# Kernel optimization log

Hardware: AMD Instinct MI355X
Metric: run time of the kernel (lower is better)

The kernel has to match this reference:

```python
import jax, jax.numpy as jnp
import numpy as np

B, T, I, H = 256, 512, 64, 256


def _lstm_layer(x, Wih, Whh, bih, bhh):
    # x: [B, T, in], Wih: [4H, in], Whh: [4H, H], biases: [4H]
    # PyTorch gate order: i, f, g, o.  c' = f*c + i*g ; h = o*tanh(c')
    Hd = Whh.shape[1]
    xp = jnp.einsum('bti,gi->btg', x, Wih) + bih + bhh  # [B, T, 4H]
    h0 = jnp.zeros((x.shape[0], Hd), x.dtype)
    c0 = jnp.zeros((x.shape[0], Hd), x.dtype)

    def step(carry, xt):
        h, c = carry
        g = xt + h @ Whh.T
        i, f, gg, o = jnp.split(g, 4, axis=-1)
        i = jax.nn.sigmoid(i)
        f = jax.nn.sigmoid(f)
        gg = jnp.tanh(gg)
        o = jax.nn.sigmoid(o)
        c = f * c + i * gg
        h = o * jnp.tanh(c)
        return (h, c), h

    _, hs = jax.lax.scan(step, (h0, c0), jnp.swapaxes(xp, 0, 1))  # [T, B, H]
    return jnp.swapaxes(hs, 0, 1)


def setup_inputs() -> dict:
    key = jax.random.key(0)
    ks = jax.random.split(key, 20)
    s_in = 1.0 / np.sqrt(I)
    s_h = 1.0 / np.sqrt(H)
    d = {
        'x': jax.random.normal(ks[0], (B, T, I), jnp.float32),
        # encoder layer 0: input I -> H
        'enc_Wih0': jax.random.normal(ks[1], (4 * H, I), jnp.float32) * s_in,
        'enc_Whh0': jax.random.normal(ks[2], (4 * H, H), jnp.float32) * s_h,
        'enc_bih0': jnp.zeros((4 * H,), jnp.float32),
        'enc_bhh0': jnp.zeros((4 * H,), jnp.float32),
        # encoder layer 1: H -> H
        'enc_Wih1': jax.random.normal(ks[3], (4 * H, H), jnp.float32) * s_h,
        'enc_Whh1': jax.random.normal(ks[4], (4 * H, H), jnp.float32) * s_h,
        'enc_bih1': jnp.zeros((4 * H,), jnp.float32),
        'enc_bhh1': jnp.zeros((4 * H,), jnp.float32),
        # decoder layer 0: H -> H
        'dec_Wih0': jax.random.normal(ks[5], (4 * H, H), jnp.float32) * s_h,
        'dec_Whh0': jax.random.normal(ks[6], (4 * H, H), jnp.float32) * s_h,
        'dec_bih0': jnp.zeros((4 * H,), jnp.float32),
        'dec_bhh0': jnp.zeros((4 * H,), jnp.float32),
        # decoder layer 1: H -> H
        'dec_Wih1': jax.random.normal(ks[7], (4 * H, H), jnp.float32) * s_h,
        'dec_Whh1': jax.random.normal(ks[8], (4 * H, H), jnp.float32) * s_h,
        'dec_bih1': jnp.zeros((4 * H,), jnp.float32),
        'dec_bhh1': jnp.zeros((4 * H,), jnp.float32),
        # output projection H -> I
        'out_W': jax.random.normal(ks[9], (I, H), jnp.float32) * s_h,
        'out_b': jnp.zeros((I,), jnp.float32),
    }
    return d


def reference(x,
              enc_Wih0, enc_Whh0, enc_bih0, enc_bhh0,
              enc_Wih1, enc_Whh1, enc_bih1, enc_bhh1,
              dec_Wih0, dec_Whh0, dec_bih0, dec_bhh0,
              dec_Wih1, dec_Whh1, dec_bih1, dec_bhh1,
              out_W, out_b):
    # Encoder (2 stacked LSTM layers, inference mode -> no inter-layer dropout)
    h = _lstm_layer(x, enc_Wih0, enc_Whh0, enc_bih0, enc_bhh0)
    encoded = _lstm_layer(h, enc_Wih1, enc_Whh1, enc_bih1, enc_bhh1)
    # Decoder (2 stacked LSTM layers over the encoded sequence)
    h = _lstm_layer(encoded, dec_Wih0, dec_Whh0, dec_bih0, dec_bhh0)
    decoded_hidden = _lstm_layer(h, dec_Wih1, dec_Whh1, dec_bih1, dec_bhh1)
    # Linear projection back to input_size
    reconstruction = jnp.einsum('bth,ih->bti', decoded_hidden, out_W) + out_b
    return reconstruction
```

## Files before the change

kernel.cpp:

```cpp
#include <hip/hip_runtime.h>

typedef unsigned short u16;
typedef unsigned int   u32;
typedef _Float16 f16;
typedef _Float16 half2v __attribute__((ext_vector_type(2)));
typedef _Float16 half8v __attribute__((ext_vector_type(8)));
typedef float float4v __attribute__((ext_vector_type(4)));

#define B_  256
#define T_  512
#define I_  64
#define H_  256
#define G_  1024
#define BT_ (B_*T_)

static __device__ __forceinline__ float fdot2u(u32 a, u32 b, float c) {
#if defined(__has_builtin) && __has_builtin(__builtin_amdgcn_fdot2)
  return __builtin_amdgcn_fdot2(__builtin_bit_cast(half2v, a),
                                __builtin_bit_cast(half2v, b), c, false);
#else
  half2v av = __builtin_bit_cast(half2v, a), bv = __builtin_bit_cast(half2v, b);
  return c + (float)av.x * (float)bv.x + (float)av.y * (float)bv.y;
#endif
}

static __device__ __forceinline__ float sig_(float x) {
  return 1.0f / (1.0f + __expf(-x));
}
static __device__ __forceinline__ float tanh_(float x) {
  float ax = fminf(fabsf(x), 15.0f);
  float e  = __expf(2.0f * ax);
  float t  = (e - 1.0f) / (e + 1.0f);
  return copysignf(t, x);
}


__global__ void cvt_f16(const float* __restrict__ in, u16* __restrict__ out, int n) {
  int i = blockIdx.x * blockDim.x + threadIdx.x;
  if (i < n) out[i] = __builtin_bit_cast(u16, (f16)in[i]);
}

__global__ void split_w(const float* __restrict__ w, u16* __restrict__ hi,
                        u16* __restrict__ lo, int n) {
  int i = blockIdx.x * blockDim.x + threadIdx.x;
  if (i < n) {
    float v = w[i];
    f16 h = (f16)v;
    float r = v - (float)h;
    hi[i] = __builtin_bit_cast(u16, h);
    lo[i] = __builtin_bit_cast(u16, (f16)r);
  }
}

__global__ void bias_sum(const float* __restrict__ a, const float* __restrict__ b,
                         float* __restrict__ o, int n) {
  int i = blockIdx.x * blockDim.x + threadIdx.x;
  if (i < n) o[i] = a[i] + b[i];
}

template<int BN>
__global__ __launch_bounds__(256) void gemm_ws(
    const u16* __restrict__ A, const u16* __restrict__ Bh, const u16* __restrict__ Bl,
    const float* __restrict__ bias, float* __restrict__ C,
    int K, int tcl, int t0, int N)
{
  constexpr int BM = 128, BK = 64, LDT = 72;
  __shared__ u16 As[BM * LDT];
  __shared__ u16 Bhs[BN * LDT];
  __shared__ u16 Bls[BN * LDT];
  const int tid = threadIdx.x, wave = tid >> 6, lane = tid & 63;
  const int m0 = blockIdx.x * BM, n0 = blockIdx.y * BN;
  constexpr int WNT = BN / 32;
  const int wm0 = (wave >> 1) * 64, wn0 = (wave & 1) * (BN / 2);
  const int tcmask = (1 << tcl) - 1;
  float4v acc[4][WNT];
  for (int i = 0; i < 4; i++)
    for (int j = 0; j < WNT; j++) acc[i][j] = (float4v){0.f, 0.f, 0.f, 0.f};
  const int lrow = lane & 15, lk = (lane >> 4) * 8;

  for (int k0 = 0; k0 < K; k0 += BK) {
    __syncthreads();
#pragma unroll
    for (int i = 0; i < 4; i++) {
      int idx = tid + i * 256, row = idx >> 3, u = idx & 7;
      int m = m0 + row;
      int rg = (m >> tcl) * T_ + t0 + (m & tcmask);
      *(uint4*)(As + row * LDT + u * 8) =
          *(const uint4*)(A + (size_t)rg * K + k0 + u * 8);
    }
#pragma unroll
    for (int i = 0; i < WNT; i++) {
      int idx = tid + i * 256, row = idx >> 3, u = idx & 7;
      size_t go = (size_t)(n0 + row) * K + k0 + u * 8;
      *(uint4*)(Bhs + row * LDT + u * 8) = *(const uint4*)(Bh + go);
      *(uint4*)(Bls + row * LDT + u * 8) = *(const uint4*)(Bl + go);
    }
    __syncthreads();
#pragma unroll
    for (int ks = 0; ks < 2; ++ks) {
      int col = ks * 32 + lk;
      half8v af[4];
#pragma unroll
      for (int mt = 0; mt < 4; mt++)
        af[mt] = *(const half8v*)(const void*)(As + (wm0 + mt * 16 + lrow) * LDT + col);
#pragma unroll
      for (int nt = 0; nt < WNT; nt++) {
        half8v bhv = *(const half8v*)(const void*)(Bhs + (wn0 + nt * 16 + lrow) * LDT + col);
        half8v blv = *(const half8v*)(const void*)(Bls + (wn0 + nt * 16 + lrow) * LDT + col);
#pragma unroll
        for (int mt = 0; mt < 4; mt++) {
          acc[mt][nt] = __builtin_amdgcn_mfma_f32_16x16x32_f16(af[mt], bhv, acc[mt][nt], 0, 0, 0);
          acc[mt][nt] = __builtin_amdgcn_mfma_f32_16x16x32_f16(af[mt], blv, acc[mt][nt], 0, 0, 0);
        }
      }
    }
  }
  const int crow = (lane >> 4) * 4, ccol = lane & 15;
#pragma unroll
  for (int nt = 0; nt < WNT; nt++) {
    int n = n0 + wn0 + nt * 16 + ccol;
    float bv = bias[n];
#pragma unroll
    for (int mt = 0; mt < 4; mt++) {
#pragma unroll
      for (int r = 0; r < 4; r++) {
        int m = m0 + wm0 + mt * 16 + crow + r;
        C[(size_t)m * N + n] = acc[mt][nt][r] + bv;
      }
    }
  }
}

__global__ __launch_bounds__(512, 2) void lstm_scan(
    const u16* __restrict__ whh, const float* __restrict__ xp,
    u16* __restrict__ hout, float* __restrict__ cst, u16* __restrict__ hst,
    int Tc, int t0)
{
  __shared__ u16 wt[1024 * 72];
  __shared__ float gs[1024];
  __shared__ u32 h2s[128];
  const int tid = threadIdx.x, b = blockIdx.x;
  const int r0 = tid, r1 = tid + 512;

  uint4 w0q[24], w1q[24];
  const uint4* g0 = (const uint4*)(whh + (size_t)r0 * 256);
  const uint4* g1 = (const uint4*)(whh + (size_t)r1 * 256);
#pragma unroll
  for (int i = 0; i < 24; i++) { w0q[i] = g0[i]; w1q[i] = g1[i]; }
#pragma unroll
  for (int i = 0; i < 8; i++) {
    *((uint4*)(wt + (size_t)r0 * 72) + i) = g0[24 + i];
    *((uint4*)(wt + (size_t)r1 * 72) + i) = g1[24 + i];
  }

  float cc = 0.f;
  if (t0 == 0) {
    if (tid < 128) h2s[tid] = 0u;
  } else {
    if (tid < 256) cc = cst[(size_t)b * 256 + tid];
    if (tid < 128) h2s[tid] = ((const u32*)hst)[(size_t)b * 128 + tid];
  }
  __syncthreads();

  const float* xpb = xp + (size_t)b * Tc * 1024;
  float xn0 = xpb[r0], xn1 = xpb[r1];
  u16* houtb = hout + (size_t)b * T_ * 256 + (size_t)t0 * 256;

  for (int tt = 0; tt < Tc; ++tt) {
    float a0 = xn0, a1 = xn1;
    if (tt + 1 < Tc) {
      xn0 = xpb[(size_t)(tt + 1) * 1024 + r0];
      xn1 = xpb[(size_t)(tt + 1) * 1024 + r1];
    }
    const uint4* hq = (const uint4*)h2s;
#pragma unroll
    for (int kc = 0; kc < 24; ++kc) {
      uint4 hv = hq[kc];
      uint4 w0 = w0q[kc], w1 = w1q[kc];
      a0 = fdot2u(w0.x, hv.x, a0); a0 = fdot2u(w0.y, hv.y, a0);
      a0 = fdot2u(w0.z, hv.z, a0); a0 = fdot2u(w0.w, hv.w, a0);
      a1 = fdot2u(w1.x, hv.x, a1); a1 = fdot2u(w1.y, hv.y, a1);
      a1 = fdot2u(w1.z, hv.z, a1); a1 = fdot2u(w1.w, hv.w, a1);
    }
    const uint4* wt0 = (const uint4*)(wt + (size_t)r0 * 72);
    const uint4* wt1 = (const uint4*)(wt + (size_t)r1 * 72);
#pragma unroll
    for (int kc = 0; kc < 8; ++kc) {
      uint4 hv = hq[24 + kc];
      uint4 w0 = wt0[kc], w1 = wt1[kc];
      a0 = fdot2u(w0.x, hv.x, a0); a0 = fdot2u(w0.y, hv.y, a0);
      a0 = fdot2u(w0.z, hv.z, a0); a0 = fdot2u(w0.w, hv.w, a0);
      a1 = fdot2u(w1.x, hv.x, a1); a1 = fdot2u(w1.y, hv.y, a1);
      a1 = fdot2u(w1.z, hv.z, a1); a1 = fdot2u(w1.w, hv.w, a1);
    }
    gs[r0] = a0; gs[r1] = a1;
    __syncthreads();
    if (tid < 256) {
      float gi = gs[tid], gf = gs[tid + 256], gg = gs[tid + 512], go = gs[tid + 768];
      float iv = sig_(gi), fv = sig_(gf), ov = sig_(go), gv = tanh_(gg);
      cc = fv * cc + iv * gv;
      float hv = ov * tanh_(cc);
      u16 hb = __builtin_bit_cast(u16, (f16)hv);
      ((u16*)h2s)[tid] = hb;
      houtb[(size_t)tt * 256 + tid] = hb;
    }
    __syncthreads();
  }
  if (tid < 256) cst[(size_t)b * 256 + tid] = cc;
  if (tid < 128) ((u32*)hst)[(size_t)b * 128 + tid] = h2s[tid];
}


extern "C" void kernel_launch(void* const* d_in, const int* in_sizes, int n_in,
                              void* d_out, int out_size, void* d_ws, size_t ws_size,
                              hipStream_t stream)
{
  const float* x      = (const float*)d_in[0];
  const float* Wih[4] = {(const float*)d_in[1], (const float*)d_in[5],
                         (const float*)d_in[9], (const float*)d_in[13]};
  const float* Whh[4] = {(const float*)d_in[2], (const float*)d_in[6],
                         (const float*)d_in[10], (const float*)d_in[14]};
  const float* bi[4]  = {(const float*)d_in[3], (const float*)d_in[7],
                         (const float*)d_in[11], (const float*)d_in[15]};
  const float* bh[4]  = {(const float*)d_in[4], (const float*)d_in[8],
                         (const float*)d_in[12], (const float*)d_in[16]};
  const float* outW   = (const float*)d_in[17];
  const float* outb   = (const float*)d_in[18];

  char* ws = (char*)d_ws;
  size_t off = 0;
  auto alc = [&](size_t bytes) -> char* {
    char* p = ws + off;
    off = (off + bytes + 255) & ~(size_t)255;
    return p;
  };

  u16* xf  = (u16*)alc((size_t)BT_ * I_ * 2);
  u16* hb0 = (u16*)alc((size_t)BT_ * H_ * 2);
  u16* hb1 = (u16*)alc((size_t)BT_ * H_ * 2);
  int wihn[4] = {G_ * I_, G_ * H_, G_ * H_, G_ * H_};
  u16 *wihH[4], *wihL[4], *whhH[4];
  float* bsum[4];
  for (int l = 0; l < 4; l++) {
    wihH[l] = (u16*)alc((size_t)wihn[l] * 2);
    wihL[l] = (u16*)alc((size_t)wihn[l] * 2);
    whhH[l] = (u16*)alc((size_t)G_ * H_ * 2);
    bsum[l] = (float*)alc((size_t)G_ * 4);
  }
  u16* owH = (u16*)alc((size_t)I_ * H_ * 2);
  u16* owL = (u16*)alc((size_t)I_ * H_ * 2);
  float* cst = (float*)alc((size_t)B_ * H_ * 4);
  u16*   hst = (u16*)alc((size_t)B_ * H_ * 2);

  int Tc = T_;
  while (Tc > 16 && off + (size_t)B_ * Tc * G_ * 4 + 4096 > ws_size) Tc >>= 1;
  float* xpb = (float*)alc((size_t)B_ * Tc * G_ * 4);
  int tcl = 0;
  while ((1 << tcl) < Tc) tcl++;

  {
    int n = BT_ * I_;
    cvt_f16<<<dim3((n + 255) / 256), dim3(256), 0, stream>>>(x, xf, n);
  }
  for (int l = 0; l < 4; l++) {
    split_w<<<dim3((wihn[l] + 255) / 256), dim3(256), 0, stream>>>(Wih[l], wihH[l], wihL[l], wihn[l]);
    cvt_f16<<<dim3((G_ * H_ + 255) / 256), dim3(256), 0, stream>>>(Whh[l], whhH[l], G_ * H_);
    bias_sum<<<dim3(4), dim3(256), 0, stream>>>(bi[l], bh[l], bsum[l], G_);
  }
  split_w<<<dim3((I_ * H_ + 255) / 256), dim3(256), 0, stream>>>(outW, owH, owL, I_ * H_);

  for (int l = 0; l < 4; l++) {
    const u16* Ain = (l == 0) ? xf : ((l == 1) ? hb0 : (l == 2) ? hb1 : hb0);
    u16* Hout = (l & 1) ? hb1 : hb0;
    int K = (l == 0) ? I_ : H_;
    for (int t0 = 0; t0 < T_; t0 += Tc) {
      gemm_ws<128><<<dim3((B_ * Tc) / 128, G_ / 128), dim3(256), 0, stream>>>(
          Ain, wihH[l], wihL[l], bsum[l], xpb, K, tcl, t0, G_);
      lstm_scan<<<dim3(B_), dim3(512), 0, stream>>>(whhH[l], xpb, Hout, cst, hst, Tc, t0);
    }
  }

  gemm_ws<64><<<dim3(BT_ / 128, 1), dim3(256), 0, stream>>>(
      hb1, owH, owL, outb, (float*)d_out, H_, 9, 0, I_);
}
```

Baseline: 4.944 ms.

## Remap gate rows to lane pairs, exchange via shuffle, double-buffer h

Reassigns Whh rows so each pair of adjacent threads holds all four gates (i,f,g,o) of one hidden unit, so gate values are exchanged with a lane shuffle instead of a shared-memory gate buffer. This removes one __syncthreads per timestep. The h vector is double-buffered in shared memory so the next step's reads do not race with this step's writes. The launch bound minimum blocks per CU is lowered from 2 to 1, which gives the compiler more register room but may reduce occupancy.

```diff
diff --git a/kernel.cpp b/kernel.cpp
--- a/kernel.cpp
+++ b/kernel.cpp
@@ -131,48 +131,52 @@
   }
 }
 
-__global__ __launch_bounds__(512, 2) void lstm_scan(
+__global__ __launch_bounds__(512, 1) void lstm_scan(
     const u16* __restrict__ whh, const float* __restrict__ xp,
     u16* __restrict__ hout, float* __restrict__ cst, u16* __restrict__ hst,
     int Tc, int t0)
 {
   __shared__ u16 wt[1024 * 72];
-  __shared__ float gs[1024];
-  __shared__ u32 h2s[128];
+  __shared__ u32 h2s[2][128];
   const int tid = threadIdx.x, b = blockIdx.x;
-  const int r0 = tid, r1 = tid + 512;
+  const int m = tid >> 1;
+  const int rA = m + (tid & 1) * 512;
+  const int rB = rA + 256;
 
   uint4 w0q[24], w1q[24];
-  const uint4* g0 = (const uint4*)(whh + (size_t)r0 * 256);
-  const uint4* g1 = (const uint4*)(whh + (size_t)r1 * 256);
+  const uint4* g0 = (const uint4*)(whh + (size_t)rA * 256);
+  const uint4* g1 = (const uint4*)(whh + (size_t)rB * 256);
 #pragma unroll
   for (int i = 0; i < 24; i++) { w0q[i] = g0[i]; w1q[i] = g1[i]; }
 #pragma unroll
   for (int i = 0; i < 8; i++) {
-    *((uint4*)(wt + (size_t)r0 * 72) + i) = g0[24 + i];
-    *((uint4*)(wt + (size_t)r1 * 72) + i) = g1[24 + i];
+    *((uint4*)(wt + (size_t)rA * 72) + i) = g0[24 + i];
+    *((uint4*)(wt + (size_t)rB * 72) + i) = g1[24 + i];
   }
 
   float cc = 0.f;
   if (t0 == 0) {
-    if (tid < 128) h2s[tid] = 0u;
+    if (tid < 128) h2s[0][tid] = 0u;
   } else {
-    if (tid < 256) cc = cst[(size_t)b * 256 + tid];
-    if (tid < 128) h2s[tid] = ((const u32*)hst)[(size_t)b * 128 + tid];
+    if (!(tid & 1)) cc = cst[(size_t)b * 256 + m];
+    if (tid < 128) h2s[0][tid] = ((const u32*)hst)[(size_t)b * 128 + tid];
   }
   __syncthreads();
 
   const float* xpb = xp + (size_t)b * Tc * 1024;
-  float xn0 = xpb[r0], xn1 = xpb[r1];
+  float xn0 = xpb[rA], xn1 = xpb[rB];
   u16* houtb = hout + (size_t)b * T_ * 256 + (size_t)t0 * 256;
+  const uint4* wt0 = (const uint4*)(wt + (size_t)rA * 72);
+  const uint4* wt1 = (const uint4*)(wt + (size_t)rB * 72);
 
   for (int tt = 0; tt < Tc; ++tt) {
+    const int rp = tt & 1, wp = rp ^ 1;
     float a0 = xn0, a1 = xn1;
     if (tt + 1 < Tc) {
-      xn0 = xpb[(size_t)(tt + 1) * 1024 + r0];
-      xn1 = xpb[(size_t)(tt + 1) * 1024 + r1];
-    }
-    const uint4* hq = (const uint4*)h2s;
+      xn0 = xpb[(size_t)(tt + 1) * 1024 + rA];
+      xn1 = xpb[(size_t)(tt + 1) * 1024 + rB];
+    }
+    const uint4* hq = (const uint4*)h2s[rp];
 #pragma unroll
     for (int kc = 0; kc < 24; ++kc) {
       uint4 hv = hq[kc];
@@ -182,8 +186,6 @@
       a1 = fdot2u(w1.x, hv.x, a1); a1 = fdot2u(w1.y, hv.y, a1);
       a1 = fdot2u(w1.z, hv.z, a1); a1 = fdot2u(w1.w, hv.w, a1);
     }
-    const uint4* wt0 = (const uint4*)(wt + (size_t)r0 * 72);
-    const uint4* wt1 = (const uint4*)(wt + (size_t)r1 * 72);
 #pragma unroll
     for (int kc = 0; kc < 8; ++kc) {
       uint4 hv = hq[24 + kc];
@@ -193,21 +195,20 @@
       a1 = fdot2u(w1.x, hv.x, a1); a1 = fdot2u(w1.y, hv.y, a1);
       a1 = fdot2u(w1.z, hv.z, a1); a1 = fdot2u(w1.w, hv.w, a1);
     }
-    gs[r0] = a0; gs[r1] = a1;
-    __syncthreads();
-    if (tid < 256) {
-      float gi = gs[tid], gf = gs[tid + 256], gg = gs[tid + 512], go = gs[tid + 768];
-      float iv = sig_(gi), fv = sig_(gf), ov = sig_(go), gv = tanh_(gg);
+    float o0 = __shfl_xor(a0, 1);
+    float o1 = __shfl_xor(a1, 1);
+    if (!(tid & 1)) {
+      float iv = sig_(a0), fv = sig_(a1), gv = tanh_(o0), ov = sig_(o1);
       cc = fv * cc + iv * gv;
       float hv = ov * tanh_(cc);
       u16 hb = __builtin_bit_cast(u16, (f16)hv);
-      ((u16*)h2s)[tid] = hb;
-      houtb[(size_t)tt * 256 + tid] = hb;
+      ((u16*)h2s[wp])[m] = hb;
+      houtb[(size_t)tt * 256 + m] = hb;
     }
     __syncthreads();
   }
-  if (tid < 256) cst[(size_t)b * 256 + tid] = cc;
-  if (tid < 128) ((u32*)hst)[(size_t)b * 128 + tid] = h2s[tid];
+  if (!(tid & 1)) cst[(size_t)b * 256 + m] = cc;
+  if (tid < 128) ((u32*)hst)[(size_t)b * 128 + tid] = h2s[Tc & 1][tid];
 }
 
 
```

Result: slower. 5.688 ms (+15.1%).
